# Kernel tuning notes

Hardware: AMD Instinct MI355X
Metric: run time of the kernel (lower is better)

Reference implementation:

```python
import jax, jax.numpy as jnp
import numpy as np

N, D_IN, D_LAT, D_FEAT, K = 12000, 64, 16, 64, 16


def setup_inputs() -> dict:
    key = jax.random.key(0)
    ks = jax.random.split(key, 7)
    s_in = 1.0 / np.sqrt(D_IN)
    s_cat = 1.0 / np.sqrt(2 * D_FEAT)
    return {
        "x": jax.random.normal(ks[0], (N, D_IN), dtype=jnp.float32),
        "W_feat": jax.random.uniform(ks[1], (D_IN, D_FEAT), jnp.float32, -s_in, s_in),
        "b_feat": jax.random.uniform(ks[2], (D_FEAT,), jnp.float32, -s_in, s_in),
        "W_lat": jax.random.uniform(ks[3], (D_IN, D_LAT), jnp.float32, -s_in, s_in),
        "b_lat": jax.random.uniform(ks[4], (D_LAT,), jnp.float32, -s_in, s_in),
        "W_out": jax.random.uniform(ks[5], (2 * D_FEAT, D_FEAT), jnp.float32, -s_cat, s_cat),
        "b_out": jax.random.uniform(ks[6], (D_FEAT,), jnp.float32, -s_cat, s_cat),
    }


def reference(x, W_feat, b_feat, W_lat, b_lat, W_out, b_out):
    # dense encoders
    feats = jnp.tanh(x @ W_feat + b_feat)      # [N, F] learned features
    coords = jnp.tanh(x @ W_lat + b_lat)       # [N, S] latent coordinates
    n = coords.shape[0]
    # full pairwise squared euclidean distances (as the module's cdist)
    sq = jnp.sum(coords * coords, axis=1)
    d2 = sq[:, None] + sq[None, :] - 2.0 * (coords @ coords.T)   # [N, N]
    d2 = jnp.maximum(d2, 0.0)
    # knn_graph: k nearest neighbors, excluding self (loop=False)
    d2_masked = jnp.where(jnp.eye(n, dtype=bool), jnp.inf, d2)
    neg_d2, idx = jax.lax.top_k(-d2_masked, K)                   # idx: [N, K] neighbor (source) ids
    edge_d2 = -neg_d2                                            # squared dist to each neighbor
    # gaussian kernel on euclidean distance: w = exp(-d^2)
    w = jnp.exp(-edge_d2)                                        # [N, K]
    # message = w * x_j, aggr='add': out_i = sum_k w_ik * feats[idx_ik]
    agg = jnp.einsum('nk,nkf->nf', w, feats[idx])                # [N, F]
    # cat self features with aggregated messages, final dense
    out = jnp.concatenate([feats, agg], axis=1) @ W_out + b_out  # [N, F]
    return out
```

## Files before the change

### kernel.cpp

```cpp
#include <hip/hip_runtime.h>
#include <math.h>

typedef unsigned long long u64;
typedef _Float16 f16x8 __attribute__((ext_vector_type(8)));
typedef float f32x16 __attribute__((ext_vector_type(16)));

#define N_PTS 12000
#define KNN 16
#define QB 16
#define NWAVES 8
#define NGROUPS32 (N_PTS / 32)
#define TAU_PTS 4096
#define TAU_GROUPS32 (TAU_PTS / 32)
#define CAP 384
#define MARGIN 0.08f
#define EVICT_KEY ((u64)0x7F400000u << 32)

__global__ __launch_bounds__(256) void encoder_kernel(
    const float* __restrict__ x, const float* __restrict__ Wf, const float* __restrict__ bf,
    const float* __restrict__ Wl, const float* __restrict__ bl,
    float* __restrict__ feats, float* __restrict__ coords, _Float16* __restrict__ coords_h,
    float* __restrict__ sq)
{
  const int wave = threadIdx.x >> 6;
  const int lane = threadIdx.x & 63;
  const int i = blockIdx.x * 4 + wave;
  if (i >= N_PTS) return;
  float xv = x[i * 64 + lane];
  float accf0 = bf[lane], accf1 = 0.0f;
  float accc0 = bl[lane & 15], accc1 = 0.0f;
  #pragma unroll
  for (int k = 0; k < 64; k += 2) {
    const float xk0 = __shfl(xv, k);
    const float xk1 = __shfl(xv, k + 1);
    accf0 = fmaf(xk0, Wf[k * 64 + lane], accf0);
    accf1 = fmaf(xk1, Wf[(k + 1) * 64 + lane], accf1);
    accc0 = fmaf(xk0, Wl[k * 16 + (lane & 15)], accc0);
    accc1 = fmaf(xk1, Wl[(k + 1) * 16 + (lane & 15)], accc1);
  }
  feats[i * 64 + lane] = tanhf(accf0 + accf1);
  float c = tanhf(accc0 + accc1);
  float cc = (lane < 16) ? c * c : 0.0f;
  cc += __shfl_xor(cc, 1);
  cc += __shfl_xor(cc, 2);
  cc += __shfl_xor(cc, 4);
  cc += __shfl_xor(cc, 8);
  if (lane < 16) {
    coords[i * 16 + lane] = c;
    coords_h[i * 16 + lane] = (_Float16)c;
  }
  if (lane == 0) sq[i] = cc;
}

__device__ __forceinline__ void ins6(u64 key, u64* k6, u64& kmax) {
  const u64 om = (key < kmax) ? kmax : ~0ull;
  #pragma unroll
  for (int t = 0; t < 6; ++t)
    k6[t] = (k6[t] == om) ? key : k6[t];
  u64 a = k6[0] > k6[1] ? k6[0] : k6[1];
  u64 b = k6[2] > k6[3] ? k6[2] : k6[3];
  u64 c = k6[4] > k6[5] ? k6[4] : k6[5];
  a = a > b ? a : b;
  kmax = a > c ? a : c;
}

__device__ __forceinline__ void ins8(u64 key, u64* k8, u64& kmax) {
  const u64 om = (key < kmax) ? kmax : ~0ull;
  #pragma unroll
  for (int t = 0; t < 8; ++t)
    k8[t] = (k8[t] == om) ? key : k8[t];
  u64 a = k8[0] > k8[1] ? k8[0] : k8[1];
  u64 b = k8[2] > k8[3] ? k8[2] : k8[3];
  u64 c = k8[4] > k8[5] ? k8[4] : k8[5];
  u64 d = k8[6] > k8[7] ? k8[6] : k8[7];
  a = a > b ? a : b;
  c = c > d ? c : d;
  kmax = a > c ? a : c;
}

__device__ __forceinline__ u64 shflx_u64(u64 v, int off) {
  int lo = __shfl_xor((int)(unsigned)v, off);
  int hi = __shfl_xor((int)(unsigned)(v >> 32), off);
  return ((u64)(unsigned)hi << 32) | (unsigned)lo;
}

__device__ __forceinline__ u64 minbfly(u64 m) {
  #pragma unroll
  for (int off = 32; off >= 1; off >>= 1) {
    u64 o = shflx_u64(m, off);
    m = (o < m) ? o : m;
  }
  return m;
}

#define CAS6(i, j) { const u64 a_ = k6[i], b_ = k6[j]; const bool sw_ = a_ > b_; \
                     k6[i] = sw_ ? b_ : a_; k6[j] = sw_ ? a_ : b_; }

#define LOADG(g, uu, ss) { const int jl_ = (g) * 32 + mcol; \
  uu = *(const uint4*)((const char*)coords_h + (size_t)jl_ * 32 + half * 16); \
  ss = sq[jl_]; }

__global__ __launch_bounds__(512, 6) void knn_agg_kernel(
    const float* __restrict__ coords, const _Float16* __restrict__ coords_h,
    const float* __restrict__ sq, const float* __restrict__ feats,
    const float* __restrict__ Wo, const float* __restrict__ bo,
    float* __restrict__ out, int* __restrict__ flags)
{
  __shared__ unsigned short sbuf[QB][CAP];
  __shared__ int scnt[QB];
  __shared__ unsigned colminS[QB][64];
  __shared__ float taugS[QB];
  __shared__ __align__(16) float featS[QB][64];
  __shared__ __align__(16) float aggS[QB][64];

  const int tid = threadIdx.x;
  const int lane = tid & 63;
  const int wave = tid >> 6;
  const int qbase = blockIdx.x * QB;
  const int mcol = lane & 31;
  const int half = lane >> 5;

  if (tid < QB) scnt[tid] = 0;
  #pragma unroll
  for (int t = tid; t < QB * 64; t += 512)
    ((unsigned*)colminS)[t] = 0x7F800000u;

  f16x8 afrag = {0, 0, 0, 0, 0, 0, 0, 0};
  if (mcol < QB) {
    const uint4 u = *(const uint4*)((const char*)coords_h + (qbase + mcol) * 32 + half * 16);
    afrag = __builtin_bit_cast(f16x8, u);
  }
  float nhsqi8[8];
  #pragma unroll
  for (int blk = 0; blk < 2; ++blk) {
    const float4 v = *(const float4*)&sq[qbase + blk * 8 + 4 * half];
    nhsqi8[blk * 4 + 0] = -0.5f * v.x; nhsqi8[blk * 4 + 1] = -0.5f * v.y;
    nhsqi8[blk * 4 + 2] = -0.5f * v.z; nhsqi8[blk * 4 + 3] = -0.5f * v.w;
  }

  f32x16 acc;
  #pragma unroll
  for (int t = 0; t < 16; ++t) acc[t] = 0.0f;

  __syncthreads();

  const int g_self = qbase >> 5;
  float lmax8[8] = {-INFINITY, -INFINITY, -INFINITY, -INFINITY,
                    -INFINITY, -INFINITY, -INFINITY, -INFINITY};
  {
    uint4 pu; float ps;
    LOADG(wave, pu, ps);
    for (int k = 0; k < 16; ++k) {
      const int g = wave + k * NWAVES;
      const uint4 cu = pu; const float cs = ps;
      const int kn = (k + 1 < 16) ? (k + 1) : 0;
      LOADG(wave + kn * NWAVES, pu, ps);

      const f16x8 bfrag = __builtin_bit_cast(f16x8, cu);
      #pragma unroll
      for (int r = 0; r < 8; ++r) acc[r] = fmaf(-0.5f, cs, nhsqi8[r]);
      acc = __builtin_amdgcn_mfma_f32_32x32x16_f16(afrag, bfrag, acc, 0, 0, 0);
      if (g == g_self) {
        #pragma unroll
        for (int r = 0; r < 8; ++r) {
          const int row = (r >> 2) * 8 + 4 * half + (r & 3);
          if (g * 32 + mcol == qbase + row) acc[r] = -INFINITY;
        }
      }
      #pragma unroll
      for (int r = 0; r < 8; ++r) lmax8[r] = fmaxf(lmax8[r], acc[r]);
    }
  }
  {
    const int cell = mcol * 2 + (wave >> 2);
    #pragma unroll
    for (int r = 0; r < 8; ++r) {
      const int row = (r >> 2) * 8 + 4 * half + (r & 3);
      atomicMin(&colminS[row][cell], __float_as_uint(fmaxf(-2.0f * lmax8[r], 0.0f)));
    }
  }
  __syncthreads();

  #pragma unroll
  for (int s = 0; s < 2; ++s) {
    const int q = wave * 2 + s;
    float v = __uint_as_float(colminS[q][lane]);
    #pragma unroll
    for (int k = 2; k <= 64; k <<= 1) {
      #pragma unroll
      for (int st = k >> 1; st >= 1; st >>= 1) {
        const float o = __shfl_xor(v, st);
        const bool keepMin = (((lane & st) == 0) == ((lane & k) == 0));
        const float mn = fminf(v, o), mx = fmaxf(v, o);
        v = keepMin ? mn : mx;
      }
    }
    const float tq = __shfl(v, 15) + MARGIN;
    if (lane == 0) taugS[q] = tq;
  }
  __syncthreads();

  float nht8[8];
  #pragma unroll
  for (int r = 0; r < 8; ++r)
    nht8[r] = -0.5f * taugS[(r >> 2) * 8 + 4 * half + (r & 3)];

  {
    uint4 pu; float ps;
    LOADG(wave, pu, ps);
    for (int g = wave; g < NGROUPS32; g += NWAVES) {
      const uint4 cu = pu; const float cs = ps;
      int gn = g + NWAVES;
      if (gn >= NGROUPS32) gn = wave;
      LOADG(gn, pu, ps);

      const f16x8 bfrag = __builtin_bit_cast(f16x8, cu);
      #pragma unroll
      for (int r = 0; r < 8; ++r) acc[r] = fmaf(-0.5f, cs, nhsqi8[r]);
      acc = __builtin_amdgcn_mfma_f32_32x32x16_f16(afrag, bfrag, acc, 0, 0, 0);
      const int j0 = g * 32;
      #pragma unroll
      for (int r = 0; r < 8; ++r) {
        if (acc[r] >= nht8[r]) {
          const int row = (r >> 2) * 8 + 4 * half + (r & 3);
          const int p = atomicAdd(&scnt[row], 1);
          if (p < CAP) sbuf[row][p] = (unsigned short)(j0 + mcol);
        }
      }
    }
  }
  __syncthreads();

  #pragma unroll
  for (int s = 0; s < 2; ++s) {
    const int lq = wave * 2 + s;
    const int qg = qbase + lq;
    const int cq = scnt[lq];
    const int nread = (cq < CAP) ? cq : CAP;
    const int nit = (nread + 63) >> 6;

    float ci[16];
    {
      const float4* cp = (const float4*)(coords + qg * 16);
      *(float4*)&ci[0] = cp[0]; *(float4*)&ci[4] = cp[1];
      *(float4*)&ci[8] = cp[2]; *(float4*)&ci[12] = cp[3];
    }
    const float sqiq = sq[qg];

    u64 k6[6];
    #pragma unroll
    for (int t = 0; t < 6; ++t) k6[t] = ((u64)(0x7F000000u + t) << 32);
    u64 kmax6 = ((u64)0x7F000005u << 32);

    for (int t = 0; t < nit; ++t) {
      const int idx = t * 64 + lane;
      u64 key = ~0ull;
      if (idx < nread) {
        const int jj = sbuf[lq][idx];
        if (jj != qg) {
          const float4* cp = (const float4*)(coords + jj * 16);
          float dot = 0.0f;
          {
            const float4 c0 = cp[0], c1 = cp[1];
            dot = fmaf(ci[0], c0.x, dot); dot = fmaf(ci[1], c0.y, dot);
            dot = fmaf(ci[2], c0.z, dot); dot = fmaf(ci[3], c0.w, dot);
            dot = fmaf(ci[4], c1.x, dot); dot = fmaf(ci[5], c1.y, dot);
            dot = fmaf(ci[6], c1.z, dot); dot = fmaf(ci[7], c1.w, dot);
          }
          {
            const float4 c2 = cp[2], c3 = cp[3];
            dot = fmaf(ci[8],  c2.x, dot); dot = fmaf(ci[9],  c2.y, dot);
            dot = fmaf(ci[10], c2.z, dot); dot = fmaf(ci[11], c2.w, dot);
            dot = fmaf(ci[12], c3.x, dot); dot = fmaf(ci[13], c3.y, dot);
            dot = fmaf(ci[14], c3.z, dot); dot = fmaf(ci[15], c3.w, dot);
          }
          const float d2 = fmaxf(fmaf(-2.0f, dot, sqiq + sq[jj]), 0.0f);
          key = ((u64)__float_as_uint(d2) << 32) | (unsigned)jj;
        }
      }
      ins6(key, k6, kmax6);
    }

    CAS6(0,5) CAS6(1,3) CAS6(2,4)
    CAS6(1,2) CAS6(3,4)
    CAS6(0,3) CAS6(2,5)
    CAS6(0,1) CAS6(2,3) CAS6(4,5)
    CAS6(1,2) CAS6(3,4)

    float dmin = __uint_as_float((unsigned)(k6[0] >> 32));
    int jmin = (int)(unsigned)(k6[0] & 0xFFFFFFFFull);

    float dv[16]; int jv[16];
    #pragma unroll
    for (int r = 0; r < KNN; ++r) {
      float m = dmin;
      #pragma unroll
      for (int off = 32; off >= 1; off >>= 1)
        m = fminf(m, __shfl_xor(m, off));
      const u64 bal = __ballot(dmin == m);
      const int owner = __ffsll((unsigned long long)bal) - 1;
      jv[r] = __builtin_amdgcn_readlane(jmin, owner);
      dv[r] = __uint_as_float(__builtin_amdgcn_readfirstlane(__float_as_uint(m)));
      const bool me = (lane == owner);
      k6[0] = me ? k6[1] : k6[0];
      k6[1] = me ? k6[2] : k6[1];
      k6[2] = me ? k6[3] : k6[2];
      k6[3] = me ? k6[4] : k6[3];
      k6[4] = me ? k6[5] : k6[4];
      k6[5] = me ? EVICT_KEY : k6[5];
      dmin = __uint_as_float((unsigned)(k6[0] >> 32));
      jmin = (int)(unsigned)(k6[0] & 0xFFFFFFFFull);
    }

    float aggv = 0.0f;
    #pragma unroll
    for (int r = 0; r < KNN; ++r)
      aggv = fmaf(__expf(-dv[r]), feats[jv[r] * 64 + lane], aggv);

    aggS[lq][lane] = aggv;
    featS[lq][lane] = feats[qg * 64 + lane];
    if (lane == 0) flags[qg] = (cq > CAP);
  }

  __syncthreads();
  const int row = tid >> 5;
  const int c2 = (tid & 31) * 2;
  float acc0 = bo[c2], acc1 = bo[c2 + 1];
  #pragma unroll
  for (int f0 = 0; f0 < 64; f0 += 4) {
    const float4 fv = *(const float4*)&featS[row][f0];
    const float4 av = *(const float4*)&aggS[row][f0];
    #pragma unroll
    for (int u = 0; u < 4; ++u) {
      const float fvu = (u == 0) ? fv.x : (u == 1) ? fv.y : (u == 2) ? fv.z : fv.w;
      const float avu = (u == 0) ? av.x : (u == 1) ? av.y : (u == 2) ? av.z : av.w;
      const float2 w0 = *(const float2*)&Wo[(f0 + u) * 64 + c2];
      const float2 w1 = *(const float2*)&Wo[(64 + f0 + u) * 64 + c2];
      acc0 = fmaf(fvu, w0.x, acc0); acc0 = fmaf(avu, w1.x, acc0);
      acc1 = fmaf(fvu, w0.y, acc1); acc1 = fmaf(avu, w1.y, acc1);
    }
  }
  const int orow = qbase + row;
  *(float2*)&out[orow * 64 + c2] = make_float2(acc0, acc1);
}

__global__ __launch_bounds__(256) void knn_fixup_kernel(
    const float* __restrict__ coords, const float* __restrict__ sq,
    const float* __restrict__ feats, const int* __restrict__ flags,
    const float* __restrict__ Wo, const float* __restrict__ bo,
    float* __restrict__ out)
{
  const int wave = threadIdx.x >> 6;
  const int lane = threadIdx.x & 63;
  for (int i = blockIdx.x * 4 + wave; i < N_PTS; i += 188) {
  if (!flags[i]) continue;
  float ci[16];
  #pragma unroll
  for (int d = 0; d < 16; ++d) ci[d] = coords[i * 16 + d];
  const float sqi = sq[i];

  u64 k8a[8], k8b[8], kmaxA, kmaxB;
  #pragma unroll
  for (int t = 0; t < 8; ++t) {
    k8a[t] = ((u64)(0x7F000000u + t) << 32);
    k8b[t] = ((u64)(0x7F000000u + t) << 32);
  }
  kmaxA = ((u64)0x7F000007u << 32);
  kmaxB = ((u64)0x7F000007u << 32);

  const int niter = (N_PTS + 63) / 64;
  for (int t = 0; t < niter; ++t) {
    const int j = t * 64 + lane;
    float4 c0 = make_float4(0,0,0,0), c1 = c0, c2 = c0, c3 = c0;
    float sqj = 0.0f;
    if (j < N_PTS) {
      const float4* cp = (const float4*)(coords + j * 16);
      c0 = cp[0]; c1 = cp[1]; c2 = cp[2]; c3 = cp[3];
      sqj = sq[j];
    }
    float dot = ci[0]*c0.x + ci[1]*c0.y + ci[2]*c0.z + ci[3]*c0.w
              + ci[4]*c1.x + ci[5]*c1.y + ci[6]*c1.z + ci[7]*c1.w
              + ci[8]*c2.x + ci[9]*c2.y + ci[10]*c2.z + ci[11]*c2.w
              + ci[12]*c3.x + ci[13]*c3.y + ci[14]*c3.z + ci[15]*c3.w;
    float d2 = fmaxf(fmaf(-2.0f, dot, sqi + sqj), 0.0f);
    const unsigned hi = (j == i || j >= N_PTS) ? 0xFFFFFFFFu : __float_as_uint(d2);
    const u64 key = ((u64)hi << 32) | (unsigned)j;
    if (t & 1) ins8(key, k8a, kmaxA);
    else       ins8(key, k8b, kmaxB);
  }

  u64 tab[16];
  #pragma unroll
  for (int t = 0; t < 8; ++t) { tab[t] = k8a[t]; tab[8 + t] = k8b[t]; }
  u64 lmin = tab[0];
  #pragma unroll
  for (int t = 1; t < 16; ++t) lmin = (tab[t] < lmin) ? tab[t] : lmin;

  float aggv = 0.0f;
  u64 T16 = 0;
  for (int r = 0; r < KNN; ++r) {
    const u64 m = minbfly(lmin);
    if (lmin == m) {
      #pragma unroll
      for (int t = 0; t < 16; ++t) tab[t] = (tab[t] == m) ? ~0ull : tab[t];
      lmin = tab[0];
      #pragma unroll
      for (int t = 1; t < 16; ++t) lmin = (tab[t] < lmin) ? tab[t] : lmin;
    }
    const unsigned hi = (unsigned)(m >> 32);
    const bool ok = hi < 0x7F000000u;
    const float w = ok ? expf(-__uint_as_float(hi)) : 0.0f;
    const int jj = ok ? (int)(unsigned)(m & 0xFFFFFFFFull) : 0;
    aggv = fmaf(w, feats[jj * 64 + lane], aggv);
    T16 = m;
  }

  if (__any((kmaxA < T16) || (kmaxB < T16))) {
    aggv = 0.0f;
    u64 prev = 0;
    for (int r = 0; r < KNN; ++r) {
      u64 best = ~0ull;
      for (int j = lane; j < N_PTS; j += 64) {
        float dot = 0.0f;
        #pragma unroll
        for (int d = 0; d < 16; ++d) dot = fmaf(ci[d], coords[j * 16 + d], dot);
        const float d2 = fmaxf(fmaf(-2.0f, dot, sqi + sq[j]), 0.0f);
        const unsigned hi = (j == i) ? 0xFFFFFFFFu : __float_as_uint(d2);
        const u64 key = ((u64)hi << 32) | (unsigned)j;
        const bool cand = (r == 0) || (key > prev);
        if (cand && key < best) best = key;
      }
      const u64 m = minbfly(best);
      prev = m;
      const unsigned hi = (unsigned)(m >> 32);
      const bool ok = hi < 0x7F000000u;
      const float w = ok ? expf(-__uint_as_float(hi)) : 0.0f;
      const int jj = ok ? (int)(unsigned)(m & 0xFFFFFFFFull) : 0;
      aggv = fmaf(w, feats[jj * 64 + lane], aggv);
    }
  }

  const float fl = feats[i * 64 + lane];
  float accv = bo[lane];
  #pragma unroll
  for (int f = 0; f < 64; ++f) {
    accv = fmaf(__shfl(fl, f),   Wo[f * 64 + lane],        accv);
    accv = fmaf(__shfl(aggv, f), Wo[(64 + f) * 64 + lane], accv);
  }
  out[i * 64 + lane] = accv;
  }
}

extern "C" void kernel_launch(void* const* d_in, const int* in_sizes, int n_in,
                              void* d_out, int out_size, void* d_ws, size_t ws_size,
                              hipStream_t stream) {
  const float* x  = (const float*)d_in[0];
  const float* Wf = (const float*)d_in[1];
  const float* bf = (const float*)d_in[2];
  const float* Wl = (const float*)d_in[3];
  const float* bl = (const float*)d_in[4];
  const float* Wo = (const float*)d_in[5];
  const float* bo = (const float*)d_in[6];
  float* out = (float*)d_out;

  char* ws = (char*)d_ws;
  float*     feats    = (float*)(ws);
  float*     coords   = (float*)(ws + 3072000);
  float*     sqv      = (float*)(ws + 3840000);
  _Float16*  coords_h = (_Float16*)(ws + 3888000);
  int*       flags    = (int*)(ws + 4272000);

  encoder_kernel<<<3000, 256, 0, stream>>>(x, Wf, bf, Wl, bl, feats, coords, coords_h, sqv);
  knn_agg_kernel<<<N_PTS / QB, 512, 0, stream>>>(coords, coords_h, sqv, feats, Wo, bo, out, flags);
  knn_fixup_kernel<<<47, 256, 0, stream>>>(coords, sqv, feats, flags, Wo, bo, out);
}
```

Baseline: 183.9 us.

## Use full 32-row MFMA tiles per block and fast tanh in encoder

```diff
diff --git a/kernel.cpp b/kernel.cpp
--- a/kernel.cpp
+++ b/kernel.cpp
@@ -7,7 +7,7 @@
 
 #define N_PTS 12000
 #define KNN 16
-#define QB 16
+#define QB 32
 #define NWAVES 8
 #define NGROUPS32 (N_PTS / 32)
 #define TAU_PTS 4096
@@ -15,6 +15,11 @@
 #define CAP 384
 #define MARGIN 0.08f
 #define EVICT_KEY ((u64)0x7F400000u << 32)
+
+__device__ __forceinline__ float fast_tanh(float v) {
+  const float e = __expf(2.0f * v);
+  return 1.0f - 2.0f * __builtin_amdgcn_rcpf(e + 1.0f);
+}
 
 __global__ __launch_bounds__(256) void encoder_kernel(
     const float* __restrict__ x, const float* __restrict__ Wf, const float* __restrict__ bf,
@@ -26,20 +31,17 @@
   const int lane = threadIdx.x & 63;
   const int i = blockIdx.x * 4 + wave;
   if (i >= N_PTS) return;
-  float xv = x[i * 64 + lane];
-  float accf0 = bf[lane], accf1 = 0.0f;
-  float accc0 = bl[lane & 15], accc1 = 0.0f;
-  #pragma unroll
-  for (int k = 0; k < 64; k += 2) {
-    const float xk0 = __shfl(xv, k);
-    const float xk1 = __shfl(xv, k + 1);
-    accf0 = fmaf(xk0, Wf[k * 64 + lane], accf0);
-    accf1 = fmaf(xk1, Wf[(k + 1) * 64 + lane], accf1);
-    accc0 = fmaf(xk0, Wl[k * 16 + (lane & 15)], accc0);
-    accc1 = fmaf(xk1, Wl[(k + 1) * 16 + (lane & 15)], accc1);
-  }
-  feats[i * 64 + lane] = tanhf(accf0 + accf1);
-  float c = tanhf(accc0 + accc1);
+  const unsigned xb = __float_as_uint(x[i * 64 + lane]);
+  float accf = bf[lane];
+  float accc = bl[lane & 15];
+  #pragma unroll
+  for (int k = 0; k < 64; ++k) {
+    const float xk = __uint_as_float(__builtin_amdgcn_readlane(xb, k));
+    accf = fmaf(xk, Wf[k * 64 + lane], accf);
+    accc = fmaf(xk, Wl[k * 16 + (lane & 15)], accc);
+  }
+  feats[i * 64 + lane] = fast_tanh(accf);
+  float c = fast_tanh(accc);
   float cc = (lane < 16) ? c * c : 0.0f;
   cc += __shfl_xor(cc, 1);
   cc += __shfl_xor(cc, 2);
@@ -100,7 +102,7 @@
   uu = *(const uint4*)((const char*)coords_h + (size_t)jl_ * 32 + half * 16); \
   ss = sq[jl_]; }
 
-__global__ __launch_bounds__(512, 6) void knn_agg_kernel(
+__global__ __launch_bounds__(512, 4) void knn_agg_kernel(
     const float* __restrict__ coords, const _Float16* __restrict__ coords_h,
     const float* __restrict__ sq, const float* __restrict__ feats,
     const float* __restrict__ Wo, const float* __restrict__ bo,
@@ -110,8 +112,8 @@
   __shared__ int scnt[QB];
   __shared__ unsigned colminS[QB][64];
   __shared__ float taugS[QB];
-  __shared__ __align__(16) float featS[QB][64];
-  __shared__ __align__(16) float aggS[QB][64];
+  __shared__ __align__(16) float featS[QB][68];
+  __shared__ __align__(16) float aggS[QB][68];
 
   const int tid = threadIdx.x;
   const int lane = tid & 63;
@@ -125,17 +127,17 @@
   for (int t = tid; t < QB * 64; t += 512)
     ((unsigned*)colminS)[t] = 0x7F800000u;
 
-  f16x8 afrag = {0, 0, 0, 0, 0, 0, 0, 0};
-  if (mcol < QB) {
+  f16x8 afrag;
+  {
     const uint4 u = *(const uint4*)((const char*)coords_h + (qbase + mcol) * 32 + half * 16);
     afrag = __builtin_bit_cast(f16x8, u);
   }
-  float nhsqi8[8];
-  #pragma unroll
-  for (int blk = 0; blk < 2; ++blk) {
+  float nhsqi[16];
+  #pragma unroll
+  for (int blk = 0; blk < 4; ++blk) {
     const float4 v = *(const float4*)&sq[qbase + blk * 8 + 4 * half];
-    nhsqi8[blk * 4 + 0] = -0.5f * v.x; nhsqi8[blk * 4 + 1] = -0.5f * v.y;
-    nhsqi8[blk * 4 + 2] = -0.5f * v.z; nhsqi8[blk * 4 + 3] = -0.5f * v.w;
+    nhsqi[blk * 4 + 0] = -0.5f * v.x; nhsqi[blk * 4 + 1] = -0.5f * v.y;
+    nhsqi[blk * 4 + 2] = -0.5f * v.z; nhsqi[blk * 4 + 3] = -0.5f * v.w;
   }
 
   f32x16 acc;
@@ -144,9 +146,10 @@
 
   __syncthreads();
 
-  const int g_self = qbase >> 5;
-  float lmax8[8] = {-INFINITY, -INFINITY, -INFINITY, -INFINITY,
-                    -INFINITY, -INFINITY, -INFINITY, -INFINITY};
+  const int g_self = blockIdx.x;
+  float lmax[16];
+  #pragma unroll
+  for (int r = 0; r < 16; ++r) lmax[r] = -INFINITY;
   {
     uint4 pu; float ps;
     LOADG(wave, pu, ps);
@@ -158,32 +161,31 @@
 
       const f16x8 bfrag = __builtin_bit_cast(f16x8, cu);
       #pragma unroll
-      for (int r = 0; r < 8; ++r) acc[r] = fmaf(-0.5f, cs, nhsqi8[r]);
+      for (int r = 0; r < 16; ++r) acc[r] = fmaf(-0.5f, cs, nhsqi[r]);
       acc = __builtin_amdgcn_mfma_f32_32x32x16_f16(afrag, bfrag, acc, 0, 0, 0);
       if (g == g_self) {
         #pragma unroll
-        for (int r = 0; r < 8; ++r) {
-          const int row = (r >> 2) * 8 + 4 * half + (r & 3);
+        for (int r = 0; r < 16; ++r) {
+          const int row = 8 * (r >> 2) + 4 * half + (r & 3);
           if (g * 32 + mcol == qbase + row) acc[r] = -INFINITY;
         }
       }
       #pragma unroll
-      for (int r = 0; r < 8; ++r) lmax8[r] = fmaxf(lmax8[r], acc[r]);
+      for (int r = 0; r < 16; ++r) lmax[r] = fmaxf(lmax[r], acc[r]);
     }
   }
   {
     const int cell = mcol * 2 + (wave >> 2);
     #pragma unroll
-    for (int r = 0; r < 8; ++r) {
-      const int row = (r >> 2) * 8 + 4 * half + (r & 3);
-      atomicMin(&colminS[row][cell], __float_as_uint(fmaxf(-2.0f * lmax8[r], 0.0f)));
+    for (int r = 0; r < 16; ++r) {
+      const int row = 8 * (r >> 2) + 4 * half + (r & 3);
+      atomicMin(&colminS[row][cell], __float_as_uint(fmaxf(-2.0f * lmax[r], 0.0f)));
     }
   }
   __syncthreads();
 
-  #pragma unroll
-  for (int s = 0; s < 2; ++s) {
-    const int q = wave * 2 + s;
+  for (int s = 0; s < 4; ++s) {
+    const int q = wave * 4 + s;
     float v = __uint_as_float(colminS[q][lane]);
     #pragma unroll
     for (int k = 2; k <= 64; k <<= 1) {
@@ -200,10 +202,10 @@
   }
   __syncthreads();
 
-  float nht8[8];
-  #pragma unroll
-  for (int r = 0; r < 8; ++r)
-    nht8[r] = -0.5f * taugS[(r >> 2) * 8 + 4 * half + (r & 3)];
+  float nht[16];
+  #pragma unroll
+  for (int r = 0; r < 16; ++r)
+    nht[r] = -0.5f * taugS[8 * (r >> 2) + 4 * half + (r & 3)];
 
   {
     uint4 pu; float ps;
@@ -216,13 +218,13 @@
 
       const f16x8 bfrag = __builtin_bit_cast(f16x8, cu);
       #pragma unroll
-      for (int r = 0; r < 8; ++r) acc[r] = fmaf(-0.5f, cs, nhsqi8[r]);
+      for (int r = 0; r < 16; ++r) acc[r] = fmaf(-0.5f, cs, nhsqi[r]);
       acc = __builtin_amdgcn_mfma_f32_32x32x16_f16(afrag, bfrag, acc, 0, 0, 0);
       const int j0 = g * 32;
       #pragma unroll
-      for (int r = 0; r < 8; ++r) {
-        if (acc[r] >= nht8[r]) {
-          const int row = (r >> 2) * 8 + 4 * half + (r & 3);
+      for (int r = 0; r < 16; ++r) {
+        if (acc[r] >= nht[r]) {
+          const int row = 8 * (r >> 2) + 4 * half + (r & 3);
           const int p = atomicAdd(&scnt[row], 1);
           if (p < CAP) sbuf[row][p] = (unsigned short)(j0 + mcol);
         }
@@ -231,9 +233,8 @@
   }
   __syncthreads();
 
-  #pragma unroll
-  for (int s = 0; s < 2; ++s) {
-    const int lq = wave * 2 + s;
+  for (int s = 0; s < 4; ++s) {
+    const int lq = wave * 4 + s;
     const int qg = qbase + lq;
     const int cq = scnt[lq];
     const int nread = (cq < CAP) ? cq : CAP;
@@ -323,9 +324,10 @@
   }
 
   __syncthreads();
-  const int row = tid >> 5;
-  const int c2 = (tid & 31) * 2;
-  float acc0 = bo[c2], acc1 = bo[c2 + 1];
+  const int row = tid >> 4;
+  const int c4 = (tid & 15) * 4;
+  float4 o;
+  o.x = bo[c4]; o.y = bo[c4 + 1]; o.z = bo[c4 + 2]; o.w = bo[c4 + 3];
   #pragma unroll
   for (int f0 = 0; f0 < 64; f0 += 4) {
     const float4 fv = *(const float4*)&featS[row][f0];
@@ -334,14 +336,15 @@
     for (int u = 0; u < 4; ++u) {
       const float fvu = (u == 0) ? fv.x : (u == 1) ? fv.y : (u == 2) ? fv.z : fv.w;
       const float avu = (u == 0) ? av.x : (u == 1) ? av.y : (u == 2) ? av.z : av.w;
-      const float2 w0 = *(const float2*)&Wo[(f0 + u) * 64 + c2];
-      const float2 w1 = *(const float2*)&Wo[(64 + f0 + u) * 64 + c2];
-      acc0 = fmaf(fvu, w0.x, acc0); acc0 = fmaf(avu, w1.x, acc0);
-      acc1 = fmaf(fvu, w0.y, acc1); acc1 = fmaf(avu, w1.y, acc1);
-    }
-  }
-  const int orow = qbase + row;
-  *(float2*)&out[orow * 64 + c2] = make_float2(acc0, acc1);
+      const float4 w0 = *(const float4*)&Wo[(f0 + u) * 64 + c4];
+      const float4 w1 = *(const float4*)&Wo[(64 + f0 + u) * 64 + c4];
+      o.x = fmaf(fvu, w0.x, o.x); o.x = fmaf(avu, w1.x, o.x);
+      o.y = fmaf(fvu, w0.y, o.y); o.y = fmaf(avu, w1.y, o.y);
+      o.z = fmaf(fvu, w0.z, o.z); o.z = fmaf(avu, w1.z, o.z);
+      o.w = fmaf(fvu, w0.w, o.w); o.w = fmaf(avu, w1.w, o.w);
+    }
+  }
+  *(float4*)&out[(qbase + row) * 64 + c4] = o;
 }
 
 __global__ __launch_bounds__(256) void knn_fixup_kernel(
```

Result: slower. 193.2 us (+5.1%).
